# Kernel tuning notes

Measured on AMD Instinct MI355X. Metric: run time of the kernel, lower is better.

Reference implementation:

```python
import jax, jax.numpy as jnp
import numpy as np

B, S, T, H, E = 256, 512, 16, 1024, 512  # batch, src_len, trg_steps, hidden, emb_dim


def setup_inputs() -> dict:
    key = jax.random.key(0)
    ks = jax.random.split(key, 10)
    rn = lambda k, sh: jax.random.normal(k, sh, dtype=jnp.float32) * 0.05
    return {
        "trg_emb": rn(ks[0], (B, T, E)),
        "h0": rn(ks[1], (B, H)),
        "c0": rn(ks[2], (B, H)),
        "ctx": rn(ks[3], (B, S, H)),
        "src_len": jax.random.randint(ks[4], (B,), 1, S + 1, dtype=jnp.int32),
        "W_ih": rn(ks[5], (4 * H, E + H)),  # input-feeding: lstm in = emb + hidden
        "W_hh": rn(ks[6], (4 * H, H)),
        "b_ih": jnp.zeros((4 * H,), jnp.float32),
        "b_hh": jnp.zeros((4 * H,), jnp.float32),
        "W_in": rn(ks[7], (H, H)),    # attention linear_in (no bias)
        "W_out": rn(ks[8], (H, 2 * H)),  # attention linear_out (no bias)
    }


def reference(trg_emb, h0, c0, ctx, src_len, W_ih, W_hh, b_ih, b_hh, W_in, W_out):
    # mask[b, s] = s < src_len[b]
    mask = jnp.arange(S)[None, :] < src_len[:, None]  # (B, S)
    neg = jnp.float32(-1e9)

    def step(carry, emb_t):
        h, c, h_tilde = carry  # each (B, H); emb_t (B, E)
        # input feeding: concat target embedding with previous attentional vector
        x = jnp.concatenate([emb_t, h_tilde], axis=1)  # (B, E+H)
        gates = x @ W_ih.T + b_ih + h @ W_hh.T + b_hh  # (B, 4H), pytorch gate order i,f,g,o
        i, f, g, o = jnp.split(gates, 4, axis=1)
        i = jax.nn.sigmoid(i); f = jax.nn.sigmoid(f)
        g = jnp.tanh(g);       o = jax.nn.sigmoid(o)
        c = f * c + i * g
        h = o * jnp.tanh(c)
        # Luong soft-dot attention with src_len masking
        target = h @ W_in.T                                # (B, H)
        scores = jnp.einsum('bsh,bh->bs', ctx, target)     # (B, S)
        scores = jnp.where(mask, scores, neg)
        attn = jax.nn.softmax(scores, axis=-1)
        weighted = jnp.einsum('bs,bsh->bh', attn, ctx)     # (B, H)
        h_tilde = jnp.tanh(jnp.concatenate([weighted, h], axis=1) @ W_out.T)
        return (h, c, h_tilde), h_tilde

    # initial h_tilde = init_hidden[0] (per the original code)
    (h_f, c_f, _), hs = jax.lax.scan(step, (h0, c0, h0), jnp.swapaxes(trg_emb, 0, 1))
    output = jnp.swapaxes(hs, 0, 1)  # (B, T, H)
    return output, h_f, c_f
```

## Files before the change

kernel.cpp:

```cpp
#include <hip/hip_runtime.h>
#include <cstdint>
#include <cstddef>


#define B_ 256
#define S_ 512
#define T_ 16
#define H_ 1024
#define E_ 512

typedef unsigned short u16;
using short8 = __attribute__((ext_vector_type(8))) short;
using f32x4  = __attribute__((ext_vector_type(4))) float;

__device__ __forceinline__ float bf2f(u16 u) {
  union { uint32_t i; float f; } v; v.i = ((uint32_t)u) << 16; return v.f;
}
__device__ __forceinline__ u16 f2bf(float f) {
  union { uint32_t i; float f; } v; v.f = f;
  uint32_t r = v.i + 0x7fffu + ((v.i >> 16) & 1u);
  return (u16)(r >> 16);
}
__device__ __forceinline__ float sigmoidf_(float x) { return 1.f / (1.f + __expf(-x)); }

__device__ __forceinline__ void gload_lds16(const void* g, void* l) {
  __builtin_amdgcn_global_load_lds(
      (const __attribute__((address_space(1))) void*)g,
      (__attribute__((address_space(3))) void*)l, 16, 0, 0);
}

__global__ __launch_bounds__(256) void cvt_bf16(const float4* __restrict__ src,
                                                ushort4* __restrict__ dst, int n4) {
  for (int i = blockIdx.x * 256 + threadIdx.x; i < n4; i += gridDim.x * 256) {
    float4 v = src[i];
    ushort4 o; o.x = f2bf(v.x); o.y = f2bf(v.y); o.z = f2bf(v.z); o.w = f2bf(v.w);
    dst[i] = o;
  }
}

__global__ __launch_bounds__(256) void cvt_rows_gi(const float* __restrict__ src,
                                                   u16* __restrict__ dst, int cols) {
  const int r = blockIdx.x;
  const int rp = (r & 1023) * 4 + (r >> 10);
  const float4* s4 = (const float4*)(src + (size_t)r * cols);
  ushort4* d4 = (ushort4*)(dst + (size_t)rp * cols);
  for (int c = threadIdx.x; c < (cols >> 2); c += 256) {
    float4 v = s4[c];
    ushort4 o; o.x = f2bf(v.x); o.y = f2bf(v.y); o.z = f2bf(v.z); o.w = f2bf(v.w);
    d4[c] = o;
  }
}

__global__ __launch_bounds__(256) void bias_gi(const float* __restrict__ b_ih,
                                               const float* __restrict__ b_hh,
                                               float* __restrict__ bsum) {
  const int r = blockIdx.x * 256 + threadIdx.x;
  const int cp = (r & 1023) * 4 + (r >> 10);
  bsum[cp] = b_ih[r] + b_hh[r];
}

__global__ __launch_bounds__(256) void init_state(const float* __restrict__ h0,
                                                  const float* __restrict__ c0,
                                                  float* __restrict__ h32,
                                                  float* __restrict__ c,
                                                  u16* __restrict__ hbf,
                                                  u16* __restrict__ htbf) {
  int idx = blockIdx.x * 256 + threadIdx.x;
  float hv = h0[idx];
  h32[idx] = hv;
  c[idx] = c0[idx];
  u16 hb = f2bf(hv);
  hbf[idx] = hb;
  htbf[idx] = hb;
}

struct Region {
  const u16* A; int lda;
  const u16* Bw; int ldb;
  int klen;
};

template <int EPI>
__global__ __launch_bounds__(256) void gemm_ms(Region r0, Region r1, Region r2, int nreg,
                                               int nmb,
                                               float* __restrict__ C, int ldc,
                                               u16* __restrict__ C2,
                                               const float* __restrict__ Ci, int cis,
                                               const float* __restrict__ bsum,
                                               float* __restrict__ cst,
                                               float* __restrict__ h32o,
                                               u16* __restrict__ hbfo) {
  __shared__ u16 smA[3][128 * 64];
  __shared__ u16 smB[3][32 * 64];
  const int tid = threadIdx.x;
  const int lane = tid & 63;
  const int wave = tid >> 6;
  const int m0 = (blockIdx.x % nmb) * 128;
  const int n0 = (blockIdx.x / nmb) * 32;

  Region rr[3] = { r0, r1, r2 };
  int tcnt[3];
  int nt = 0;
#pragma unroll
  for (int rg = 0; rg < 3; ++rg) { tcnt[rg] = (rg < nreg) ? (rr[rg].klen >> 6) : 0; nt += tcnt[rg]; }

  auto stage = [&](int lin, int buf) {
    int rg = 0, base = 0;
    while (lin >= base + tcnt[rg]) { base += tcnt[rg]; ++rg; }
    const int kr = (lin - base) << 6;
    const u16* A = rr[rg].A;  const int lda = rr[rg].lda;
    const u16* Bw = rr[rg].Bw; const int ldb = rr[rg].ldb;
#pragma unroll
    for (int j = 0; j < 4; ++j) {
      const int c = j * 256 + tid;
      const int row = c >> 3;
      const int q = (c & 7) ^ (row & 7);
      gload_lds16(A + (size_t)(m0 + row) * lda + kr + q * 8,
                  (char*)&smA[buf][0] + (size_t)(j * 256 + wave * 64) * 16);
    }
    {
      const int row = tid >> 3;
      const int q = (tid & 7) ^ (row & 7);
      gload_lds16(Bw + (size_t)(n0 + row) * ldb + kr + q * 8,
                  (char*)&smB[buf][0] + (size_t)(wave * 64) * 16);
    }
  };

  f32x4 acc[2][2] = {};
  stage(0, 0);
  if (nt > 1) stage(1, 1);
  for (int ti = 0; ti < nt; ++ti) {
    const int buf = ti % 3;
    if (ti + 2 < nt) {
      stage(ti + 2, (ti + 2) % 3);
      asm volatile("s_waitcnt vmcnt(10)" ::: "memory");
    } else if (ti + 1 < nt) {
      asm volatile("s_waitcnt vmcnt(5)" ::: "memory");
    } else {
      asm volatile("s_waitcnt vmcnt(0)" ::: "memory");
    }
    __builtin_amdgcn_s_barrier();
    const int row16 = lane & 15;
#pragma unroll
    for (int ks = 0; ks < 2; ++ks) {
      const int q = ks * 4 + (lane >> 4);
      short8 af[2], bfr[2];
#pragma unroll
      for (int mi = 0; mi < 2; ++mi) {
        const int R = wave * 32 + mi * 16 + row16;
        af[mi] = *(const short8*)((const char*)&smA[buf][0] + (size_t)(R * 8 + (q ^ (R & 7))) * 16);
      }
#pragma unroll
      for (int ni = 0; ni < 2; ++ni) {
        const int Rn = ni * 16 + row16;
        bfr[ni] = *(const short8*)((const char*)&smB[buf][0] + (size_t)(Rn * 8 + (q ^ (Rn & 7))) * 16);
      }
#pragma unroll
      for (int mi = 0; mi < 2; ++mi)
#pragma unroll
        for (int ni = 0; ni < 2; ++ni)
          acc[mi][ni] = __builtin_amdgcn_mfma_f32_16x16x32_bf16(af[mi], bfr[ni], acc[mi][ni], 0, 0, 0);
    }
    __builtin_amdgcn_s_barrier();
  }
  const int row16 = lane & 15;
  const int kg = lane >> 4;
#pragma unroll
  for (int mi = 0; mi < 2; ++mi) {
#pragma unroll
    for (int ni = 0; ni < 2; ++ni) {
#pragma unroll
      for (int r = 0; r < 4; ++r) {
        const int row = m0 + wave * 32 + mi * 16 + kg * 4 + r;
        const int col = n0 + ni * 16 + row16;
        float v = acc[mi][ni][r];
        if (EPI == 0) {
          C[(size_t)row * ldc + col] = v;
        } else if (EPI == 1) {
          C2[row * H_ + col] = f2bf(v);
        } else if (EPI == 2) {
          float tv = tanhf(v);
          C[(size_t)row * ldc + col] = tv;
          C2[row * H_ + col] = f2bf(tv);
        } else {
          v += Ci[(size_t)row * cis + col] + bsum[col];
          float v1 = __shfl_xor(v, 1);
          float v2 = __shfl_xor(v, 2);
          float v3 = __shfl_xor(v, 3);
          if ((row16 & 3) == 0) {
            const int u = (n0 + ni * 16 + (row16 & ~3)) >> 2;
            float iv = sigmoidf_(v);
            float fv = sigmoidf_(v1);
            float gv = tanhf(v2);
            float ov = sigmoidf_(v3);
            float cn = fv * cst[row * H_ + u] + iv * gv;
            float hn = ov * tanhf(cn);
            cst[row * H_ + u] = cn;
            h32o[row * H_ + u] = hn;
            hbfo[row * H_ + u] = f2bf(hn);
          }
        }
      }
    }
  }
}

template <int ISBF>
__global__ __launch_bounds__(1024) void attn_on(const void* __restrict__ ctxv,
                                                const u16* __restrict__ target,
                                                const int* __restrict__ src_len,
                                                u16* __restrict__ wbf) {
  __shared__ float facc[16][1024];
  __shared__ float fm[16], fl[16];
  const int b = blockIdx.x;
  const int tid = threadIdx.x;
  const int lane = tid & 63;
  const int wave = tid >> 6;
  const int len = src_len[b];
  float tg[16];
  {
    const u16* tp = target + b * H_ + lane * 16;
    short8 v1 = *(const short8*)tp;
    short8 v2 = *(const short8*)(tp + 8);
#pragma unroll
    for (int j = 0; j < 8; ++j) { tg[j] = bf2f((u16)v1[j]); tg[8 + j] = bf2f((u16)v2[j]); }
  }
  float m = -1e30f, l = 0.f;
  float acc[16];
#pragma unroll
  for (int j = 0; j < 16; ++j) acc[j] = 0.f;

  if (ISBF) {
    const u16* cb = (const u16*)ctxv + (size_t)b * (S_ * H_);
    int s = wave;
    short8 c1 = {}, c2 = {};
    if (s < len) {
      const u16* p = cb + (size_t)s * H_ + lane * 16;
      c1 = *(const short8*)p; c2 = *(const short8*)(p + 8);
    }
    while (s < len) {
      const int sn = s + 16;
      short8 n1 = {}, n2 = {};
      if (sn < len) {
        const u16* p = cb + (size_t)sn * H_ + lane * 16;
        n1 = *(const short8*)p; n2 = *(const short8*)(p + 8);
      }
      float cf[16];
#pragma unroll
      for (int j = 0; j < 8; ++j) { cf[j] = bf2f((u16)c1[j]); cf[8 + j] = bf2f((u16)c2[j]); }
      float x = 0.f;
#pragma unroll
      for (int j = 0; j < 16; ++j) x += cf[j] * tg[j];
#pragma unroll
      for (int off = 1; off < 64; off <<= 1) x += __shfl_xor(x, off);
      if (x > m) {
        float sc_ = __expf(m - x);
        l *= sc_;
#pragma unroll
        for (int j = 0; j < 16; ++j) acc[j] *= sc_;
        m = x;
      }
      float p = __expf(x - m);
      l += p;
#pragma unroll
      for (int j = 0; j < 16; ++j) acc[j] += p * cf[j];
      s = sn; c1 = n1; c2 = n2;
    }
  } else {
    const float* cb = (const float*)ctxv + (size_t)b * (S_ * H_);
    for (int s = wave; s < len; s += 16) {
      const float* cr = cb + (size_t)s * H_ + lane * 16;
      float cf[16];
#pragma unroll
      for (int j4 = 0; j4 < 4; ++j4) {
        float4 v = *(const float4*)(cr + j4 * 4);
        cf[j4 * 4] = v.x; cf[j4 * 4 + 1] = v.y; cf[j4 * 4 + 2] = v.z; cf[j4 * 4 + 3] = v.w;
      }
      float x = 0.f;
#pragma unroll
      for (int j = 0; j < 16; ++j) x += cf[j] * tg[j];
#pragma unroll
      for (int off = 1; off < 64; off <<= 1) x += __shfl_xor(x, off);
      if (x > m) {
        float sc_ = __expf(m - x);
        l *= sc_;
#pragma unroll
        for (int j = 0; j < 16; ++j) acc[j] *= sc_;
        m = x;
      }
      float p = __expf(x - m);
      l += p;
#pragma unroll
      for (int j = 0; j < 16; ++j) acc[j] += p * cf[j];
    }
  }
  if (lane == 0) { fm[wave] = m; fl[wave] = l; }
#pragma unroll
  for (int j4 = 0; j4 < 4; ++j4) {
    float4 v;
    v.x = acc[j4 * 4]; v.y = acc[j4 * 4 + 1]; v.z = acc[j4 * 4 + 2]; v.w = acc[j4 * 4 + 3];
    *(float4*)&facc[wave][lane * 16 + j4 * 4] = v;
  }
  __syncthreads();
  float mstar = -1e30f;
#pragma unroll
  for (int w = 0; w < 16; ++w) mstar = fmaxf(mstar, fm[w]);
  float lsum = 0.f, asum = 0.f;
#pragma unroll
  for (int w = 0; w < 16; ++w) {
    float e = __expf(fm[w] - mstar);
    lsum += fl[w] * e;
    asum += facc[w][tid] * e;
  }
  wbf[b * H_ + tid] = f2bf(asum / lsum);
}

extern "C" void kernel_launch(void* const* d_in, const int* in_sizes, int n_in,
                              void* d_out, int out_size, void* d_ws, size_t ws_size,
                              hipStream_t stream) {
  const float* trg_emb = (const float*)d_in[0];
  const float* h0      = (const float*)d_in[1];
  const float* c0      = (const float*)d_in[2];
  const float* ctx     = (const float*)d_in[3];
  const int*   src_len = (const int*)d_in[4];
  const float* W_ih    = (const float*)d_in[5];
  const float* W_hh    = (const float*)d_in[6];
  const float* b_ih    = (const float*)d_in[7];
  const float* b_hh    = (const float*)d_in[8];
  const float* W_in    = (const float*)d_in[9];
  const float* W_out   = (const float*)d_in[10];
  float* out = (float*)d_out;

  char* w = (char*)d_ws;
  u16*   wWih  = (u16*)(w);
  u16*   wWhh  = (u16*)(w + 12582912);
  u16*   wWin  = (u16*)(w + 20971520);
  u16*   wWout = (u16*)(w + 23068672);
  u16*   wemb  = (u16*)(w + 27262976);
  float* wbsum = (float*)(w + 31457280);
  float* wh32  = (float*)(w + 31473664);
  float* wc    = (float*)(w + 32522240);
  u16*   whbf  = (u16*)(w + 33570816);
  u16*   whtbf = (u16*)(w + 34095104);
  u16*   wtgt  = (u16*)(w + 34619392);
  u16*   wwbf  = (u16*)(w + 35143680);
  float* wGemb = (float*)(w + 35667968);
  u16*   wctx  = (u16*)(w + 102776832);
  const bool ctx_bf = ws_size >= (size_t)102776832 + (size_t)268435456;

  auto cvt_launch = [&](const float* s, u16* d, int n) {
    int n4 = n / 4;
    int grid = (n4 + 255) / 256;
    if (grid > 4096) grid = 4096;
    cvt_bf16<<<dim3(grid), dim3(256), 0, stream>>>((const float4*)s, (ushort4*)d, n4);
  };
  cvt_rows_gi<<<dim3(4096), dim3(256), 0, stream>>>(W_ih, wWih, 1536);
  cvt_rows_gi<<<dim3(4096), dim3(256), 0, stream>>>(W_hh, wWhh, 1024);
  bias_gi<<<dim3(16), dim3(256), 0, stream>>>(b_ih, b_hh, wbsum);
  cvt_launch(W_in,  wWin,  1024 * 1024);
  cvt_launch(W_out, wWout, 1024 * 2048);
  cvt_launch(trg_emb, wemb, B_ * T_ * E_);
  if (ctx_bf) cvt_launch(ctx, wctx, B_ * S_ * H_);
  init_state<<<dim3((B_ * H_) / 256), dim3(256), 0, stream>>>(h0, c0, wh32, wc, whbf, whtbf);

  Region dummy = { nullptr, 0, nullptr, 0, 0 };
  {
    Region e0 = { wemb, E_, wWih, E_ + H_, E_ };
    gemm_ms<0><<<dim3(32 * 128), dim3(256), 0, stream>>>(
        e0, dummy, dummy, 1, 32, wGemb, 4096, (u16*)nullptr,
        nullptr, 0, nullptr, nullptr, nullptr, nullptr);
  }

  for (int t = 0; t < T_; ++t) {
    Region g0 = { whtbf, H_, wWih + E_, E_ + H_, H_ };
    Region g1 = { whbf,  H_, wWhh,      H_,      H_ };
    gemm_ms<3><<<dim3(2 * 128), dim3(256), 0, stream>>>(
        g0, g1, dummy, 2, 2, nullptr, 0, (u16*)nullptr,
        wGemb + (size_t)t * 4096, T_ * 4096, wbsum, wc, wh32, whbf);
    Region i0 = { whbf, H_, wWin, H_, H_ };
    gemm_ms<1><<<dim3(2 * 32), dim3(256), 0, stream>>>(
        i0, dummy, dummy, 1, 2, nullptr, 0, wtgt,
        nullptr, 0, nullptr, nullptr, nullptr, nullptr);
    if (ctx_bf)
      attn_on<1><<<dim3(B_), dim3(1024), 0, stream>>>((const void*)wctx, wtgt, src_len, wwbf);
    else
      attn_on<0><<<dim3(B_), dim3(1024), 0, stream>>>((const void*)ctx, wtgt, src_len, wwbf);
    Region o0 = { wwbf, H_, wWout,      2 * H_, H_ };
    Region o1 = { whbf, H_, wWout + H_, 2 * H_, H_ };
    gemm_ms<2><<<dim3(2 * 32), dim3(256), 0, stream>>>(
        o0, o1, dummy, 2, 2, out + (size_t)t * H_, T_ * H_, whtbf,
        nullptr, 0, nullptr, nullptr, nullptr, nullptr);
  }
  hipMemcpyAsync(out + (size_t)B_ * T_ * H_, wh32, (size_t)B_ * H_ * sizeof(float),
                 hipMemcpyDeviceToDevice, stream);
  hipMemcpyAsync(out + (size_t)B_ * T_ * H_ + B_ * H_, wc, (size_t)B_ * H_ * sizeof(float),
                 hipMemcpyDeviceToDevice, stream);
}
```

Before: 2.134 ms.

## Fuse all stages into one persistent cooperative megakernel with grid syncs

Replaces the roughly 70 separate kernel launches (conversions, embedding GEMM, and four kernels per timestep) with a single cooperative kernel of 256 blocks of 1024 threads that uses grid.sync between phases. GEMM tiles become 64x64 with 16 waves per block and double buffering instead of triple, and the attention reduction adds a two-level merge of the partial softmax results. h is double-buffered across steps to avoid a read/write race within the fused step. This removes per-launch overhead and inter-kernel gaps, but every phase is now bound to one fixed grid, several GEMM phases use only 64 of 256 blocks, and each grid sync has its own cost.

```diff
diff --git a/kernel.cpp b/kernel.cpp
--- a/kernel.cpp
+++ b/kernel.cpp
@@ -1,6 +1,9 @@
 #include <hip/hip_runtime.h>
+#include <hip/hip_cooperative_groups.h>
 #include <cstdint>
 #include <cstddef>
+
+namespace cg = cooperative_groups;
 
 
 #define B_ 256
@@ -29,197 +32,125 @@
       (__attribute__((address_space(3))) void*)l, 16, 0, 0);
 }
 
-__global__ __launch_bounds__(256) void cvt_bf16(const float4* __restrict__ src,
-                                                ushort4* __restrict__ dst, int n4) {
-  for (int i = blockIdx.x * 256 + threadIdx.x; i < n4; i += gridDim.x * 256) {
-    float4 v = src[i];
-    ushort4 o; o.x = f2bf(v.x); o.y = f2bf(v.y); o.z = f2bf(v.z); o.w = f2bf(v.w);
-    dst[i] = o;
-  }
-}
-
-__global__ __launch_bounds__(256) void cvt_rows_gi(const float* __restrict__ src,
-                                                   u16* __restrict__ dst, int cols) {
-  const int r = blockIdx.x;
-  const int rp = (r & 1023) * 4 + (r >> 10);
-  const float4* s4 = (const float4*)(src + (size_t)r * cols);
-  ushort4* d4 = (ushort4*)(dst + (size_t)rp * cols);
-  for (int c = threadIdx.x; c < (cols >> 2); c += 256) {
-    float4 v = s4[c];
-    ushort4 o; o.x = f2bf(v.x); o.y = f2bf(v.y); o.z = f2bf(v.z); o.w = f2bf(v.w);
-    d4[c] = o;
-  }
-}
-
-__global__ __launch_bounds__(256) void bias_gi(const float* __restrict__ b_ih,
-                                               const float* __restrict__ b_hh,
-                                               float* __restrict__ bsum) {
-  const int r = blockIdx.x * 256 + threadIdx.x;
-  const int cp = (r & 1023) * 4 + (r >> 10);
-  bsum[cp] = b_ih[r] + b_hh[r];
-}
-
-__global__ __launch_bounds__(256) void init_state(const float* __restrict__ h0,
-                                                  const float* __restrict__ c0,
-                                                  float* __restrict__ h32,
-                                                  float* __restrict__ c,
-                                                  u16* __restrict__ hbf,
-                                                  u16* __restrict__ htbf) {
-  int idx = blockIdx.x * 256 + threadIdx.x;
-  float hv = h0[idx];
-  h32[idx] = hv;
-  c[idx] = c0[idx];
-  u16 hb = f2bf(hv);
-  hbf[idx] = hb;
-  htbf[idx] = hb;
-}
-
-struct Region {
-  const u16* A; int lda;
-  const u16* Bw; int ldb;
-  int klen;
+struct Reg2 { const u16* A; int lda; const u16* B; int ldb; int kt; };
+
+struct MegaP {
+  const float* trg_emb; const float* h0; const float* c0; const float* ctx;
+  const int* src_len;
+  const float* W_ih; const float* W_hh; const float* b_ih; const float* b_hh;
+  const float* W_in; const float* W_out;
+  float* out;
+  u16* wWih; u16* wWhh; u16* wWin; u16* wWout; u16* wemb;
+  float* wbsum; float* wh32; float* wc; float* wGemb;
+  u16* whbf0; u16* whbf1; u16* whtbf; u16* wtgt; u16* wwbf; u16* wctx;
+  int ctx_bf;
 };
 
+union SMem {
+  struct { u16 A[2][4096]; u16 B[2][4096]; } g;
+  struct { float facc[8][1024]; float fm[16]; float fl[16]; } a;
+};
+
 template <int EPI>
-__global__ __launch_bounds__(256) void gemm_ms(Region r0, Region r1, Region r2, int nreg,
-                                               int nmb,
-                                               float* __restrict__ C, int ldc,
-                                               u16* __restrict__ C2,
-                                               const float* __restrict__ Ci, int cis,
-                                               const float* __restrict__ bsum,
-                                               float* __restrict__ cst,
-                                               float* __restrict__ h32o,
-                                               u16* __restrict__ hbfo) {
-  __shared__ u16 smA[3][128 * 64];
-  __shared__ u16 smB[3][32 * 64];
-  const int tid = threadIdx.x;
+__device__ void gemm_tile(SMem* sm, const int tid, const int m0, const int n0,
+                          const Reg2 r0, const Reg2 r1,
+                          float* __restrict__ Cf, u16* __restrict__ Cb,
+                          const float* __restrict__ Ci,
+                          const float* __restrict__ bsum,
+                          float* __restrict__ cst, float* __restrict__ h32o,
+                          u16* __restrict__ hbfo, const int tstep) {
   const int lane = tid & 63;
   const int wave = tid >> 6;
-  const int m0 = (blockIdx.x % nmb) * 128;
-  const int n0 = (blockIdx.x / nmb) * 32;
-
-  Region rr[3] = { r0, r1, r2 };
-  int tcnt[3];
-  int nt = 0;
-#pragma unroll
-  for (int rg = 0; rg < 3; ++rg) { tcnt[rg] = (rg < nreg) ? (rr[rg].klen >> 6) : 0; nt += tcnt[rg]; }
-
-  auto stage = [&](int lin, int buf) {
-    int rg = 0, base = 0;
-    while (lin >= base + tcnt[rg]) { base += tcnt[rg]; ++rg; }
-    const int kr = (lin - base) << 6;
-    const u16* A = rr[rg].A;  const int lda = rr[rg].lda;
-    const u16* Bw = rr[rg].Bw; const int ldb = rr[rg].ldb;
-#pragma unroll
-    for (int j = 0; j < 4; ++j) {
-      const int c = j * 256 + tid;
-      const int row = c >> 3;
-      const int q = (c & 7) ^ (row & 7);
-      gload_lds16(A + (size_t)(m0 + row) * lda + kr + q * 8,
-                  (char*)&smA[buf][0] + (size_t)(j * 256 + wave * 64) * 16);
-    }
-    {
-      const int row = tid >> 3;
-      const int q = (tid & 7) ^ (row & 7);
-      gload_lds16(Bw + (size_t)(n0 + row) * ldb + kr + q * 8,
-                  (char*)&smB[buf][0] + (size_t)(wave * 64) * 16);
+  const int nt = r0.kt + r1.kt;
+  const int wm = ((wave >> 2) << 4);
+  const int wn = ((wave & 3) << 4);
+  const int row16 = lane & 15;
+  const int kg = lane >> 4;
+
+  auto stage = [&](int ti, int buf) {
+    const bool fst = ti < r0.kt;
+    const u16* Ap = fst ? r0.A : r1.A;
+    const u16* Bp = fst ? r0.B : r1.B;
+    const int lda = fst ? r0.lda : r1.lda;
+    const int ldb = fst ? r0.ldb : r1.ldb;
+    const int kr = (fst ? ti : ti - r0.kt) << 6;
+    if (tid < 512) {
+      const int row = tid >> 3, qs = tid & 7;
+      gload_lds16(Ap + (size_t)(m0 + row) * lda + kr + ((qs ^ (row & 7)) << 3),
+                  (char*)&sm->g.A[buf][0] + (wave << 10));
+    } else {
+      const int c = tid - 512;
+      const int row = c >> 3, qs = c & 7;
+      gload_lds16(Bp + (size_t)(n0 + row) * ldb + kr + ((qs ^ (row & 7)) << 3),
+                  (char*)&sm->g.B[buf][0] + ((wave - 8) << 10));
     }
   };
 
-  f32x4 acc[2][2] = {};
+  f32x4 acc = {0.f, 0.f, 0.f, 0.f};
   stage(0, 0);
-  if (nt > 1) stage(1, 1);
   for (int ti = 0; ti < nt; ++ti) {
-    const int buf = ti % 3;
-    if (ti + 2 < nt) {
-      stage(ti + 2, (ti + 2) % 3);
-      asm volatile("s_waitcnt vmcnt(10)" ::: "memory");
-    } else if (ti + 1 < nt) {
-      asm volatile("s_waitcnt vmcnt(5)" ::: "memory");
+    const int buf = ti & 1;
+    if (ti + 1 < nt) {
+      stage(ti + 1, buf ^ 1);
+      asm volatile("s_waitcnt vmcnt(1)" ::: "memory");
     } else {
       asm volatile("s_waitcnt vmcnt(0)" ::: "memory");
     }
     __builtin_amdgcn_s_barrier();
-    const int row16 = lane & 15;
-#pragma unroll
-    for (int ks = 0; ks < 2; ++ks) {
-      const int q = ks * 4 + (lane >> 4);
-      short8 af[2], bfr[2];
-#pragma unroll
-      for (int mi = 0; mi < 2; ++mi) {
-        const int R = wave * 32 + mi * 16 + row16;
-        af[mi] = *(const short8*)((const char*)&smA[buf][0] + (size_t)(R * 8 + (q ^ (R & 7))) * 16);
+    const int Ra = wm + row16;
+    const int Rb = wn + row16;
+    short8 a0 = *(const short8*)((const char*)&sm->g.A[buf][0] + (size_t)((Ra << 3) + (kg ^ (Ra & 7))) * 16);
+    short8 b0 = *(const short8*)((const char*)&sm->g.B[buf][0] + (size_t)((Rb << 3) + (kg ^ (Rb & 7))) * 16);
+    short8 a1 = *(const short8*)((const char*)&sm->g.A[buf][0] + (size_t)((Ra << 3) + ((4 + kg) ^ (Ra & 7))) * 16);
+    short8 b1 = *(const short8*)((const char*)&sm->g.B[buf][0] + (size_t)((Rb << 3) + ((4 + kg) ^ (Rb & 7))) * 16);
+    asm volatile("s_waitcnt lgkmcnt(0)" ::: "memory");
+    __builtin_amdgcn_sched_barrier(0);
+    acc = __builtin_amdgcn_mfma_f32_16x16x32_bf16(a0, b0, acc, 0, 0, 0);
+    acc = __builtin_amdgcn_mfma_f32_16x16x32_bf16(a1, b1, acc, 0, 0, 0);
+    __builtin_amdgcn_sched_barrier(0);
+    __builtin_amdgcn_s_barrier();
+  }
+#pragma unroll
+  for (int r = 0; r < 4; ++r) {
+    const int row = m0 + wm + (kg << 2) + r;
+    const int col = n0 + wn + row16;
+    float v = acc[r];
+    if (EPI == 0) {
+      Cf[(size_t)row * 4096 + col] = v;
+    } else if (EPI == 1) {
+      Cb[row * H_ + col] = f2bf(v);
+    } else if (EPI == 2) {
+      float tv = tanhf(v);
+      Cf[(size_t)row * (T_ * H_) + tstep * H_ + col] = tv;
+      Cb[row * H_ + col] = f2bf(tv);
+    } else {
+      v += Ci[(size_t)row * (T_ * 4096) + col] + bsum[col];
+      float v1 = __shfl_xor(v, 1);
+      float v2 = __shfl_xor(v, 2);
+      float v3 = __shfl_xor(v, 3);
+      if ((lane & 3) == 0) {
+        const int u = col >> 2;
+        float iv = sigmoidf_(v);
+        float fv = sigmoidf_(v1);
+        float gv = tanhf(v2);
+        float ov = sigmoidf_(v3);
+        float cn = fv * cst[row * H_ + u] + iv * gv;
+        float hn = ov * tanhf(cn);
+        cst[row * H_ + u] = cn;
+        h32o[row * H_ + u] = hn;
+        hbfo[row * H_ + u] = f2bf(hn);
       }
-#pragma unroll
-      for (int ni = 0; ni < 2; ++ni) {
-        const int Rn = ni * 16 + row16;
-        bfr[ni] = *(const short8*)((const char*)&smB[buf][0] + (size_t)(Rn * 8 + (q ^ (Rn & 7))) * 16);
-      }
-#pragma unroll
-      for (int mi = 0; mi < 2; ++mi)
-#pragma unroll
-        for (int ni = 0; ni < 2; ++ni)
-          acc[mi][ni] = __builtin_amdgcn_mfma_f32_16x16x32_bf16(af[mi], bfr[ni], acc[mi][ni], 0, 0, 0);
-    }
-    __builtin_amdgcn_s_barrier();
-  }
-  const int row16 = lane & 15;
-  const int kg = lane >> 4;
-#pragma unroll
-  for (int mi = 0; mi < 2; ++mi) {
-#pragma unroll
-    for (int ni = 0; ni < 2; ++ni) {
-#pragma unroll
-      for (int r = 0; r < 4; ++r) {
-        const int row = m0 + wave * 32 + mi * 16 + kg * 4 + r;
-        const int col = n0 + ni * 16 + row16;
-        float v = acc[mi][ni][r];
-        if (EPI == 0) {
-          C[(size_t)row * ldc + col] = v;
-        } else if (EPI == 1) {
-          C2[row * H_ + col] = f2bf(v);
-        } else if (EPI == 2) {
-          float tv = tanhf(v);
-          C[(size_t)row * ldc + col] = tv;
-          C2[row * H_ + col] = f2bf(tv);
-        } else {
-          v += Ci[(size_t)row * cis + col] + bsum[col];
-          float v1 = __shfl_xor(v, 1);
-          float v2 = __shfl_xor(v, 2);
-          float v3 = __shfl_xor(v, 3);
-          if ((row16 & 3) == 0) {
-            const int u = (n0 + ni * 16 + (row16 & ~3)) >> 2;
-            float iv = sigmoidf_(v);
-            float fv = sigmoidf_(v1);
-            float gv = tanhf(v2);
-            float ov = sigmoidf_(v3);
-            float cn = fv * cst[row * H_ + u] + iv * gv;
-            float hn = ov * tanhf(cn);
-            cst[row * H_ + u] = cn;
-            h32o[row * H_ + u] = hn;
-            hbfo[row * H_ + u] = f2bf(hn);
-          }
-        }
-      }
-    }
-  }
-}
-
-template <int ISBF>
-__global__ __launch_bounds__(1024) void attn_on(const void* __restrict__ ctxv,
-                                                const u16* __restrict__ target,
-                                                const int* __restrict__ src_len,
-                                                u16* __restrict__ wbf) {
-  __shared__ float facc[16][1024];
-  __shared__ float fm[16], fl[16];
-  const int b = blockIdx.x;
-  const int tid = threadIdx.x;
+    }
+  }
+}
+
+__device__ void attn_phase(SMem* sm, const MegaP& P, const int bid, const int tid) {
   const int lane = tid & 63;
   const int wave = tid >> 6;
-  const int len = src_len[b];
+  const int len = P.src_len[bid];
   float tg[16];
   {
-    const u16* tp = target + b * H_ + lane * 16;
+    const u16* tp = P.wtgt + bid * H_ + lane * 16;
     short8 v1 = *(const short8*)tp;
     short8 v2 = *(const short8*)(tp + 8);
 #pragma unroll
@@ -230,24 +161,15 @@
 #pragma unroll
   for (int j = 0; j < 16; ++j) acc[j] = 0.f;
 
-  if (ISBF) {
-    const u16* cb = (const u16*)ctxv + (size_t)b * (S_ * H_);
-    int s = wave;
-    short8 c1 = {}, c2 = {};
-    if (s < len) {
-      const u16* p = cb + (size_t)s * H_ + lane * 16;
-      c1 = *(const short8*)p; c2 = *(const short8*)(p + 8);
-    }
-    while (s < len) {
-      const int sn = s + 16;
-      short8 n1 = {}, n2 = {};
-      if (sn < len) {
-        const u16* p = cb + (size_t)sn * H_ + lane * 16;
-        n1 = *(const short8*)p; n2 = *(const short8*)(p + 8);
-      }
+  if (P.ctx_bf) {
+    const u16* cb = P.wctx + (size_t)bid * (S_ * H_);
+    for (int s = wave; s < len; s += 16) {
+      const u16* cr = cb + (size_t)s * H_ + lane * 16;
+      short8 v1 = *(const short8*)cr;
+      short8 v2 = *(const short8*)(cr + 8);
       float cf[16];
 #pragma unroll
-      for (int j = 0; j < 8; ++j) { cf[j] = bf2f((u16)c1[j]); cf[8 + j] = bf2f((u16)c2[j]); }
+      for (int j = 0; j < 8; ++j) { cf[j] = bf2f((u16)v1[j]); cf[8 + j] = bf2f((u16)v2[j]); }
       float x = 0.f;
 #pragma unroll
       for (int j = 0; j < 16; ++j) x += cf[j] * tg[j];
@@ -264,10 +186,9 @@
       l += p;
 #pragma unroll
       for (int j = 0; j < 16; ++j) acc[j] += p * cf[j];
-      s = sn; c1 = n1; c2 = n2;
     }
   } else {
-    const float* cb = (const float*)ctxv + (size_t)b * (S_ * H_);
+    const float* cb = P.ctx + (size_t)bid * (S_ * H_);
     for (int s = wave; s < len; s += 16) {
       const float* cr = cb + (size_t)s * H_ + lane * 16;
       float cf[16];
@@ -294,105 +215,195 @@
       for (int j = 0; j < 16; ++j) acc[j] += p * cf[j];
     }
   }
-  if (lane == 0) { fm[wave] = m; fl[wave] = l; }
-#pragma unroll
-  for (int j4 = 0; j4 < 4; ++j4) {
-    float4 v;
-    v.x = acc[j4 * 4]; v.y = acc[j4 * 4 + 1]; v.z = acc[j4 * 4 + 2]; v.w = acc[j4 * 4 + 3];
-    *(float4*)&facc[wave][lane * 16 + j4 * 4] = v;
+
+  if (wave >= 8) {
+#pragma unroll
+    for (int j4 = 0; j4 < 4; ++j4) {
+      float4 v;
+      v.x = acc[j4 * 4]; v.y = acc[j4 * 4 + 1]; v.z = acc[j4 * 4 + 2]; v.w = acc[j4 * 4 + 3];
+      *(float4*)&sm->a.facc[wave - 8][lane * 16 + j4 * 4] = v;
+    }
+    if (lane == 0) { sm->a.fm[wave] = m; sm->a.fl[wave] = l; }
+  }
+  __syncthreads();
+  if (wave < 8) {
+    float pm = sm->a.fm[8 + wave];
+    float pl = sm->a.fl[8 + wave];
+    float M = fmaxf(m, pm);
+    float e1 = __expf(m - M);
+    float e2 = __expf(pm - M);
+#pragma unroll
+    for (int j4 = 0; j4 < 4; ++j4) {
+      float4 pv = *(float4*)&sm->a.facc[wave][lane * 16 + j4 * 4];
+      float4 nv;
+      nv.x = acc[j4 * 4 + 0] * e1 + pv.x * e2;
+      nv.y = acc[j4 * 4 + 1] * e1 + pv.y * e2;
+      nv.z = acc[j4 * 4 + 2] * e1 + pv.z * e2;
+      nv.w = acc[j4 * 4 + 3] * e1 + pv.w * e2;
+      *(float4*)&sm->a.facc[wave][lane * 16 + j4 * 4] = nv;
+    }
+    if (lane == 0) { sm->a.fm[wave] = M; sm->a.fl[wave] = l * e1 + pl * e2; }
   }
   __syncthreads();
   float mstar = -1e30f;
 #pragma unroll
-  for (int w = 0; w < 16; ++w) mstar = fmaxf(mstar, fm[w]);
+  for (int w = 0; w < 8; ++w) mstar = fmaxf(mstar, sm->a.fm[w]);
   float lsum = 0.f, asum = 0.f;
 #pragma unroll
-  for (int w = 0; w < 16; ++w) {
-    float e = __expf(fm[w] - mstar);
-    lsum += fl[w] * e;
-    asum += facc[w][tid] * e;
-  }
-  wbf[b * H_ + tid] = f2bf(asum / lsum);
+  for (int w = 0; w < 8; ++w) {
+    float e = __expf(sm->a.fm[w] - mstar);
+    lsum += sm->a.fl[w] * e;
+    asum += sm->a.facc[w][tid] * e;
+  }
+  P.wwbf[bid * H_ + tid] = f2bf(asum / lsum);
+}
+
+__global__ __launch_bounds__(1024, 4) void mega(MegaP P) {
+  cg::grid_group grid = cg::this_grid();
+  __shared__ SMem sm;
+  const int tid = threadIdx.x;
+  const int bid = blockIdx.x;
+  const int gtid = bid * 1024 + tid;
+  const int GSZ = 256 * 1024;
+
+  for (int i = gtid; i < 4096 * 384; i += GSZ) {
+    const int r = i / 384, c4 = i - r * 384;
+    const int rp = ((r & 1023) << 2) + (r >> 10);
+    float4 v = ((const float4*)P.W_ih)[i];
+    ushort4 o; o.x = f2bf(v.x); o.y = f2bf(v.y); o.z = f2bf(v.z); o.w = f2bf(v.w);
+    ((ushort4*)P.wWih)[(size_t)rp * 384 + c4] = o;
+  }
+  for (int i = gtid; i < 4096 * 256; i += GSZ) {
+    const int r = i >> 8, c4 = i & 255;
+    const int rp = ((r & 1023) << 2) + (r >> 10);
+    float4 v = ((const float4*)P.W_hh)[i];
+    ushort4 o; o.x = f2bf(v.x); o.y = f2bf(v.y); o.z = f2bf(v.z); o.w = f2bf(v.w);
+    ((ushort4*)P.wWhh)[(size_t)rp * 256 + c4] = o;
+  }
+  {
+    float4 v = ((const float4*)P.W_in)[gtid];
+    ushort4 o; o.x = f2bf(v.x); o.y = f2bf(v.y); o.z = f2bf(v.z); o.w = f2bf(v.w);
+    ((ushort4*)P.wWin)[gtid] = o;
+  }
+  for (int i = gtid; i < 524288; i += GSZ) {
+    float4 v = ((const float4*)P.W_out)[i];
+    ushort4 o; o.x = f2bf(v.x); o.y = f2bf(v.y); o.z = f2bf(v.z); o.w = f2bf(v.w);
+    ((ushort4*)P.wWout)[i] = o;
+  }
+  for (int i = gtid; i < 524288; i += GSZ) {
+    float4 v = ((const float4*)P.trg_emb)[i];
+    ushort4 o; o.x = f2bf(v.x); o.y = f2bf(v.y); o.z = f2bf(v.z); o.w = f2bf(v.w);
+    ((ushort4*)P.wemb)[i] = o;
+  }
+  if (gtid < 4096) {
+    const int cp = ((gtid & 1023) << 2) + (gtid >> 10);
+    P.wbsum[cp] = P.b_ih[gtid] + P.b_hh[gtid];
+  }
+  {
+    float hv = P.h0[gtid];
+    P.wh32[gtid] = hv;
+    P.wc[gtid] = P.c0[gtid];
+    u16 hb = f2bf(hv);
+    P.whbf0[gtid] = hb;
+    P.whtbf[gtid] = hb;
+  }
+  if (P.ctx_bf) {
+    for (int i = gtid; i < 33554432; i += GSZ) {
+      float4 v = ((const float4*)P.ctx)[i];
+      ushort4 o; o.x = f2bf(v.x); o.y = f2bf(v.y); o.z = f2bf(v.z); o.w = f2bf(v.w);
+      ((ushort4*)P.wctx)[i] = o;
+    }
+  }
+  grid.sync();
+
+  {
+    Reg2 ra = { P.wemb, E_, P.wWih, E_ + H_, 8 };
+    Reg2 rb = { nullptr, 0, nullptr, 0, 0 };
+    for (int tile = bid; tile < 4096; tile += 256) {
+      const int m0 = (tile & 63) << 6;
+      const int n0 = (tile >> 6) << 6;
+      gemm_tile<0>(&sm, tid, m0, n0, ra, rb, P.wGemb, nullptr,
+                   nullptr, nullptr, nullptr, nullptr, nullptr, 0);
+    }
+  }
+  grid.sync();
+
+  for (int t = 0; t < T_; ++t) {
+    const u16* hcur = (t & 1) ? P.whbf1 : P.whbf0;
+    u16* hnxt = (t & 1) ? P.whbf0 : P.whbf1;
+    {
+      const int m0 = (bid & 3) << 6;
+      const int n0 = (bid >> 2) << 6;
+      Reg2 ra = { P.whtbf, H_, P.wWih + E_, E_ + H_, 16 };
+      Reg2 rb = { hcur,    H_, P.wWhh,      H_,      16 };
+      gemm_tile<3>(&sm, tid, m0, n0, ra, rb, nullptr, nullptr,
+                   P.wGemb + t * 4096, P.wbsum, P.wc, P.wh32, hnxt, 0);
+    }
+    grid.sync();
+    if (bid < 64) {
+      const int m0 = (bid & 3) << 6;
+      const int n0 = (bid >> 2) << 6;
+      Reg2 ra = { hnxt, H_, P.wWin, H_, 16 };
+      Reg2 rb = { nullptr, 0, nullptr, 0, 0 };
+      gemm_tile<1>(&sm, tid, m0, n0, ra, rb, nullptr, P.wtgt,
+                   nullptr, nullptr, nullptr, nullptr, nullptr, 0);
+    }
+    grid.sync();
+    attn_phase(&sm, P, bid, tid);
+    grid.sync();
+    if (bid < 64) {
+      const int m0 = (bid & 3) << 6;
+      const int n0 = (bid >> 2) << 6;
+      Reg2 ra = { P.wwbf, H_, P.wWout,      2 * H_, 16 };
+      Reg2 rb = { hnxt,   H_, P.wWout + H_, 2 * H_, 16 };
+      gemm_tile<2>(&sm, tid, m0, n0, ra, rb, P.out, P.whtbf,
+                   nullptr, nullptr, nullptr, nullptr, nullptr, t);
+    }
+    grid.sync();
+  }
+
+  P.out[(size_t)B_ * T_ * H_ + gtid] = P.wh32[gtid];
+  P.out[(size_t)B_ * T_ * H_ + B_ * H_ + gtid] = P.wc[gtid];
 }
 
 extern "C" void kernel_launch(void* const* d_in, const int* in_sizes, int n_in,
                               void* d_out, int out_size, void* d_ws, size_t ws_size,
                               hipStream_t stream) {
-  const float* trg_emb = (const float*)d_in[0];
-  const float* h0      = (const float*)d_in[1];
-  const float* c0      = (const float*)d_in[2];
-  const float* ctx     = (const float*)d_in[3];
-  const int*   src_len = (const int*)d_in[4];
-  const float* W_ih    = (const float*)d_in[5];
-  const float* W_hh    = (const float*)d_in[6];
-  const float* b_ih    = (const float*)d_in[7];
-  const float* b_hh    = (const float*)d_in[8];
-  const float* W_in    = (const float*)d_in[9];
-  const float* W_out   = (const float*)d_in[10];
-  float* out = (float*)d_out;
-
   char* w = (char*)d_ws;
-  u16*   wWih  = (u16*)(w);
-  u16*   wWhh  = (u16*)(w + 12582912);
-  u16*   wWin  = (u16*)(w + 20971520);
-  u16*   wWout = (u16*)(w + 23068672);
-  u16*   wemb  = (u16*)(w + 27262976);
-  float* wbsum = (float*)(w + 31457280);
-  float* wh32  = (float*)(w + 31473664);
-  float* wc    = (float*)(w + 32522240);
-  u16*   whbf  = (u16*)(w + 33570816);
-  u16*   whtbf = (u16*)(w + 34095104);
-  u16*   wtgt  = (u16*)(w + 34619392);
-  u16*   wwbf  = (u16*)(w + 35143680);
-  float* wGemb = (float*)(w + 35667968);
-  u16*   wctx  = (u16*)(w + 102776832);
-  const bool ctx_bf = ws_size >= (size_t)102776832 + (size_t)268435456;
-
-  auto cvt_launch = [&](const float* s, u16* d, int n) {
-    int n4 = n / 4;
-    int grid = (n4 + 255) / 256;
-    if (grid > 4096) grid = 4096;
-    cvt_bf16<<<dim3(grid), dim3(256), 0, stream>>>((const float4*)s, (ushort4*)d, n4);
-  };
-  cvt_rows_gi<<<dim3(4096), dim3(256), 0, stream>>>(W_ih, wWih, 1536);
-  cvt_rows_gi<<<dim3(4096), dim3(256), 0, stream>>>(W_hh, wWhh, 1024);
-  bias_gi<<<dim3(16), dim3(256), 0, stream>>>(b_ih, b_hh, wbsum);
-  cvt_launch(W_in,  wWin,  1024 * 1024);
-  cvt_launch(W_out, wWout, 1024 * 2048);
-  cvt_launch(trg_emb, wemb, B_ * T_ * E_);
-  if (ctx_bf) cvt_launch(ctx, wctx, B_ * S_ * H_);
-  init_state<<<dim3((B_ * H_) / 256), dim3(256), 0, stream>>>(h0, c0, wh32, wc, whbf, whtbf);
-
-  Region dummy = { nullptr, 0, nullptr, 0, 0 };
-  {
-    Region e0 = { wemb, E_, wWih, E_ + H_, E_ };
-    gemm_ms<0><<<dim3(32 * 128), dim3(256), 0, stream>>>(
-        e0, dummy, dummy, 1, 32, wGemb, 4096, (u16*)nullptr,
-        nullptr, 0, nullptr, nullptr, nullptr, nullptr);
-  }
-
-  for (int t = 0; t < T_; ++t) {
-    Region g0 = { whtbf, H_, wWih + E_, E_ + H_, H_ };
-    Region g1 = { whbf,  H_, wWhh,      H_,      H_ };
-    gemm_ms<3><<<dim3(2 * 128), dim3(256), 0, stream>>>(
-        g0, g1, dummy, 2, 2, nullptr, 0, (u16*)nullptr,
-        wGemb + (size_t)t * 4096, T_ * 4096, wbsum, wc, wh32, whbf);
-    Region i0 = { whbf, H_, wWin, H_, H_ };
-    gemm_ms<1><<<dim3(2 * 32), dim3(256), 0, stream>>>(
-        i0, dummy, dummy, 1, 2, nullptr, 0, wtgt,
-        nullptr, 0, nullptr, nullptr, nullptr, nullptr);
-    if (ctx_bf)
-      attn_on<1><<<dim3(B_), dim3(1024), 0, stream>>>((const void*)wctx, wtgt, src_len, wwbf);
-    else
-      attn_on<0><<<dim3(B_), dim3(1024), 0, stream>>>((const void*)ctx, wtgt, src_len, wwbf);
-    Region o0 = { wwbf, H_, wWout,      2 * H_, H_ };
-    Region o1 = { whbf, H_, wWout + H_, 2 * H_, H_ };
-    gemm_ms<2><<<dim3(2 * 32), dim3(256), 0, stream>>>(
-        o0, o1, dummy, 2, 2, out + (size_t)t * H_, T_ * H_, whtbf,
-        nullptr, 0, nullptr, nullptr, nullptr, nullptr);
-  }
-  hipMemcpyAsync(out + (size_t)B_ * T_ * H_, wh32, (size_t)B_ * H_ * sizeof(float),
-                 hipMemcpyDeviceToDevice, stream);
-  hipMemcpyAsync(out + (size_t)B_ * T_ * H_ + B_ * H_, wc, (size_t)B_ * H_ * sizeof(float),
-                 hipMemcpyDeviceToDevice, stream);
-}
+  MegaP P;
+  P.trg_emb = (const float*)d_in[0];
+  P.h0      = (const float*)d_in[1];
+  P.c0      = (const float*)d_in[2];
+  P.ctx     = (const float*)d_in[3];
+  P.src_len = (const int*)d_in[4];
+  P.W_ih    = (const float*)d_in[5];
+  P.W_hh    = (const float*)d_in[6];
+  P.b_ih    = (const float*)d_in[7];
+  P.b_hh    = (const float*)d_in[8];
+  P.W_in    = (const float*)d_in[9];
+  P.W_out   = (const float*)d_in[10];
+  P.out     = (float*)d_out;
+
+  size_t off = 0;
+  auto alloc = [&](size_t bytes) { char* p = w + off; off += bytes; return p; };
+  P.wWih  = (u16*)  alloc(12582912);
+  P.wWhh  = (u16*)  alloc(8388608);
+  P.wWin  = (u16*)  alloc(2097152);
+  P.wWout = (u16*)  alloc(4194304);
+  P.wemb  = (u16*)  alloc(4194304);
+  P.wbsum = (float*)alloc(16384);
+  P.wh32  = (float*)alloc(1048576);
+  P.wc    = (float*)alloc(1048576);
+  P.whbf0 = (u16*)  alloc(524288);
+  P.whbf1 = (u16*)  alloc(524288);
+  P.whtbf = (u16*)  alloc(524288);
+  P.wtgt  = (u16*)  alloc(524288);
+  P.wwbf  = (u16*)  alloc(524288);
+  P.wGemb = (float*)alloc(67108864);
+  size_t need_ctx = off + (size_t)268435456;
+  P.wctx  = (u16*)  alloc(268435456);
+  P.ctx_bf = (ws_size >= need_ctx) ? 1 : 0;
+
+  void* args[] = { (void*)&P };
+  hipLaunchCooperativeKernel((const void*)mega, dim3(256), dim3(1024), args, 0, stream);
+}
```

Measured after the change: 4.507 ms. 111% more time.
